# Kernel optimization log

Hardware: AMD Instinct MI355X
Metric: run time of the kernel (lower is better)

## Reference

```python
import jax, jax.numpy as jnp
import numpy as np

B, L, D = 8, 8192, 512
TARGET_RATIO = 1.0 / 6.0


def _normalize(v):
    # matches torch F.normalize(dim=-1, eps=1e-12)
    n = jnp.maximum(jnp.linalg.norm(v, axis=-1, keepdims=True), 1e-12)
    return v / n


def _downsample(x, b_hard):
    # vectorized stream compaction, padded to L (static upper bound of L_max)
    Bb, Ll, Dd = x.shape
    cnt = jnp.cumsum(b_hard.astype(jnp.int32), axis=1)
    pos = jnp.where(b_hard > 0.5, cnt - 1, Ll)          # non-selected -> dump slot L
    bidx = jnp.arange(Bb)[:, None]
    out = jnp.zeros((Bb, Ll + 1, Dd), x.dtype).at[bidx, pos].set(x)[:, :Ll]
    counts = cnt[:, -1]
    mask = jnp.arange(Ll)[None, :] < counts[:, None]
    return out, mask


def setup_inputs() -> dict:
    key = jax.random.key(0)
    k1, k2, k3 = jax.random.split(key, 3)
    x = jax.random.normal(k1, (B, L, D), jnp.float32)
    W_q = jax.random.normal(k2, (D, D), jnp.float32) / np.sqrt(D)
    W_k = jax.random.normal(k3, (D, D), jnp.float32) / np.sqrt(D)
    return {"x": x, "W_q": W_q, "W_k": W_k}


def reference(x, W_q, W_k):
    q = _normalize(jnp.einsum('bld,ed->ble', x, W_q))   # nn.Linear: x @ W.T
    k = _normalize(jnp.einsum('bld,ed->ble', x, W_k))
    k_prev = jnp.pad(k[:, :-1, :], ((0, 0), (1, 0), (0, 0)))
    cos_sim = jnp.sum(q * k_prev, axis=-1)               # (B, L)
    p = jnp.clip(0.5 * (1.0 - cos_sim), 0.0, 1.0)
    p = p.at[:, 0].set(1.0)                              # first position always boundary
    b_hard = (p >= 0.5).astype(x.dtype)
    N = 1.0 / TARGET_RATIO
    F_actual = jnp.mean(b_hard)
    G_actual = jnp.mean(p)
    ratio_loss = N / (N - 1.0) * ((N - 1.0) * F_actual * G_actual + (1.0 - F_actual) * (1.0 - G_actual))
    compressed, comp_mask = _downsample(x, b_hard)
    p_compressed, _ = _downsample(p[..., None], b_hard)
    p_compressed = p_compressed[..., 0]
    return (compressed, comp_mask, b_hard, p, p_compressed, ratio_loss)
```

## Files before the change

kernel.cpp:

```cpp
#include <hip/hip_runtime.h>
#include <hip/hip_bf16.h>
#include <math.h>

#define BB 8
#define LL 8192
#define DD 512
#define NROWS (BB * LL)

#define OUT_COMP   0
#define OUT_MASK   33554432
#define OUT_BHARD  33619968
#define OUT_P      33685504
#define OUT_PCOMP  33751040
#define OUT_LOSS   33816576

#define WS_FIXLIST 0
#define WS_FIXCNT  262144
#define WS_COUNTS  262148
#define WS_SUMP    262180
#define WS_SEL     262212
#define WS_SSK     524416
#define WS_SSQ     786560
#define WS_DOT     1048704
#define WS_WQH     1310848
#define WS_WKH     1835136

#define FIX_CAP 65536
#define FIX_TAU 1e-4f

typedef __attribute__((ext_vector_type(8))) _Float16 half8;
typedef __attribute__((ext_vector_type(4))) float f32x4;

static __device__ __forceinline__ void ld_g2l16(const void* g, void* l) {
  __builtin_amdgcn_global_load_lds(
      (const __attribute__((address_space(1))) void*)g,
      (__attribute__((address_space(3))) void*)l, 16, 0, 0);
}

__global__ __launch_bounds__(256) void wsplit(
    const float* __restrict__ Wq, const float* __restrict__ Wk,
    _Float16* __restrict__ wqh, _Float16* __restrict__ wkh,
    float* __restrict__ ssk, float* __restrict__ ssq,
    float* __restrict__ dotb, int* __restrict__ fixcnt) {
  const int t = blockIdx.x * 256 + threadIdx.x;
  if (t == 0) *fixcnt = 0;
  ssk[t] = 0.0f;
  ssq[t] = 0.0f;
  dotb[t] = 0.0f;

  const int m = t >> 15;
  const int c = t & 32767;
  const int kt = c >> 11;
  const int ct = (c >> 6) & 31;
  const int l = c & 63;
  const int n = l & 15;
  const int kblk = l >> 4;
  const int e = ct * 16 + n;
  const int d0 = kt * 32 + kblk * 8;
  const float* src = (m ? Wk : Wq) + (long)e * 512 + d0;
  _Float16* dh = (m ? wkh : wqh) + (long)c * 8;
  float4 v0 = *(const float4*)src;
  float4 v1 = *(const float4*)(src + 4);
  float av[8] = {v0.x, v0.y, v0.z, v0.w, v1.x, v1.y, v1.z, v1.w};
  half8 hi;
#pragma unroll
  for (int j = 0; j < 8; ++j) hi[j] = (_Float16)av[j];
  *(half8*)dh = hi;
}

__global__ __launch_bounds__(256, 2) void gemm_fused(
    const float* __restrict__ x,
    const _Float16* __restrict__ wqh, const _Float16* __restrict__ wkh,
    float* __restrict__ ssqOut, float* __restrict__ sskOut,
    float* __restrict__ dotOut,
    float* __restrict__ qedge, float* __restrict__ kedge) {
  __shared__ _Float16 smem[32768];
  _Float16* AH0 = smem;
  _Float16* AL0 = smem + 4096;
  _Float16* AH1 = smem + 8192;
  _Float16* AL1 = smem + 12288;
  _Float16* BQ0 = smem + 16384;
  _Float16* BK0 = smem + 20480;
  _Float16* BQ1 = smem + 24576;
  _Float16* BK1 = smem + 28672;

  const int tid = threadIdx.x;
  const int lane = tid & 63;
  const int w = tid >> 6;
  const int wrow = w & 1, wcol = w >> 1;
  const int g = lane >> 4, n = lane & 15;
  const int bx0 = blockIdx.x;
  const int bx = ((bx0 & 7) << 8) | (bx0 >> 3);
  const int rb = bx >> 2, cb = bx & 3;
  const long r0 = (long)rb * 128;

  const int arow = ((tid >> 6) << 4) | (tid & 15);
  const int akb = (tid >> 4) & 3;
  const float* ap = x + (r0 + arow) * 512 + akb * 8;

  f32x4 accq[4][4], acck[4][4];
#pragma unroll
  for (int mb = 0; mb < 4; ++mb)
#pragma unroll
    for (int nb = 0; nb < 4; ++nb) {
      accq[mb][nb] = (f32x4){0.f, 0.f, 0.f, 0.f};
      acck[mb][nb] = (f32x4){0.f, 0.f, 0.f, 0.f};
    }

#define STAGE_B(ktv, BQ_, BK_)                                              \
  do {                                                                      \
    const long bb = ((long)((ktv)*32 + cb * 8) << 9) + w * 1024 + lane * 8; \
    ld_g2l16(wqh + bb, (BQ_) + w * 1024);                                   \
    ld_g2l16(wqh + bb + 512, (BQ_) + w * 1024 + 512);                       \
    ld_g2l16(wkh + bb, (BK_) + w * 1024);                                   \
    ld_g2l16(wkh + bb + 512, (BK_) + w * 1024 + 512);                       \
  } while (0)

#define CONV_A(F0, F1, F2, F3, AH_, AL_)                                  \
  do {                                                                    \
    float av0[8] = {F0.x, F0.y, F0.z, F0.w, F1.x, F1.y, F1.z, F1.w};      \
    float av1[8] = {F2.x, F2.y, F2.z, F2.w, F3.x, F3.y, F3.z, F3.w};      \
    half8 h0, h1, l0, l1;                                                 \
    _Pragma("unroll") for (int j = 0; j < 8; ++j) {                       \
      _Float16 a = (_Float16)av0[j];                                      \
      h0[j] = a;                                                          \
      l0[j] = (_Float16)(av0[j] - (float)a);                              \
      _Float16 b = (_Float16)av1[j];                                      \
      h1[j] = b;                                                          \
      l1[j] = (_Float16)(av1[j] - (float)b);                              \
    }                                                                     \
    *(half8*)((AH_) + tid * 8) = h0;                                      \
    *(half8*)((AH_) + (tid + 256) * 8) = h1;                              \
    *(half8*)((AL_) + tid * 8) = l0;                                      \
    *(half8*)((AL_) + (tid + 256) * 8) = l1;                              \
  } while (0)

#define COMPUTE(AH_, AL_, BQ_, BK_)                                       \
  do {                                                                    \
    half8 ah[4], al[4], bq[4], bk[4];                                     \
    _Pragma("unroll") for (int nb = 0; nb < 4; ++nb) {                    \
      bq[nb] = *(const half8*)((BQ_) + ((wcol * 4 + nb) * 64 + lane) * 8);\
      bk[nb] = *(const half8*)((BK_) + ((wcol * 4 + nb) * 64 + lane) * 8);\
    }                                                                     \
    _Pragma("unroll") for (int mb = 0; mb < 4; ++mb) {                    \
      const int cm = wrow * 4 + mb;                                       \
      ah[mb] = *(const half8*)((AH_) + (cm * 64 + lane) * 8);             \
      al[mb] = *(const half8*)((AL_) + (cm * 64 + lane) * 8);             \
    }                                                                     \
    __builtin_amdgcn_s_setprio(1);                                        \
    _Pragma("unroll") for (int nb = 0; nb < 4; ++nb)                      \
        _Pragma("unroll") for (int mb = 0; mb < 4; ++mb) {                \
      accq[mb][nb] = __builtin_amdgcn_mfma_f32_16x16x32_f16(              \
          ah[mb], bq[nb], accq[mb][nb], 0, 0, 0);                         \
      acck[mb][nb] = __builtin_amdgcn_mfma_f32_16x16x32_f16(              \
          ah[mb], bk[nb], acck[mb][nb], 0, 0, 0);                         \
      accq[mb][nb] = __builtin_amdgcn_mfma_f32_16x16x32_f16(              \
          al[mb], bq[nb], accq[mb][nb], 0, 0, 0);                         \
      acck[mb][nb] = __builtin_amdgcn_mfma_f32_16x16x32_f16(              \
          al[mb], bk[nb], acck[mb][nb], 0, 0, 0);                        \
    }                                                                     \
    __builtin_amdgcn_s_setprio(0);                                        \
  } while (0)

#define BARRIER_CNT()                                       \
  do {                                                      \
    asm volatile("s_waitcnt vmcnt(4)" ::: "memory");        \
    asm volatile("s_waitcnt lgkmcnt(0)" ::: "memory");      \
    __builtin_amdgcn_sched_barrier(0);                      \
    __builtin_amdgcn_s_barrier();                           \
  } while (0)

#define FENCE() __builtin_amdgcn_sched_barrier(0)

  STAGE_B(0, BQ0, BK0);
  FENCE();
  float4 pa0 = *(const float4*)(ap);
  float4 pa1 = *(const float4*)(ap + 4);
  float4 pa2 = *(const float4*)(ap + 64 * 512);
  float4 pa3 = *(const float4*)(ap + 64 * 512 + 4);
  FENCE();
  CONV_A(pa0, pa1, pa2, pa3, AH0, AL0);
  float4 pb0 = *(const float4*)(ap + 32);
  float4 pb1 = *(const float4*)(ap + 32 + 4);
  float4 pb2 = *(const float4*)(ap + 32 + 64 * 512);
  float4 pb3 = *(const float4*)(ap + 32 + 64 * 512 + 4);
  FENCE();
  BARRIER_CNT();

  for (int i = 0; i < 8; ++i) {
    const int kt = 2 * i;
    STAGE_B(kt + 1, BQ1, BK1);
    FENCE();
    {
      const int ktn = (kt + 2 < 16) ? (kt + 2) : 15;
      const float* xp = ap + ktn * 32;
      pa0 = *(const float4*)(xp);
      pa1 = *(const float4*)(xp + 4);
      pa2 = *(const float4*)(xp + 64 * 512);
      pa3 = *(const float4*)(xp + 64 * 512 + 4);
    }
    FENCE();
    CONV_A(pb0, pb1, pb2, pb3, AH1, AL1);
    COMPUTE(AH0, AL0, BQ0, BK0);
    BARRIER_CNT();
    {
      const int ktn = (kt + 2 < 16) ? (kt + 2) : 15;
      STAGE_B(ktn, BQ0, BK0);
    }
    FENCE();
    {
      const int ktn = (kt + 3 < 16) ? (kt + 3) : 15;
      const float* xp2 = ap + ktn * 32;
      pb0 = *(const float4*)(xp2);
      pb1 = *(const float4*)(xp2 + 4);
      pb2 = *(const float4*)(xp2 + 64 * 512);
      pb3 = *(const float4*)(xp2 + 64 * 512 + 4);
    }
    FENCE();
    CONV_A(pa0, pa1, pa2, pa3, AH0, AL0);
    COMPUTE(AH1, AL1, BQ1, BK1);
    BARRIER_CNT();
  }

  asm volatile("s_waitcnt vmcnt(0)" ::: "memory");
  __builtin_amdgcn_sched_barrier(0);
  __syncthreads();

  _Float16* KX = smem;
  const int col0 = wcol * 64 + n;
  const int rbase = wrow * 64;
#pragma unroll
  for (int mb = 0; mb < 4; ++mb)
#pragma unroll
    for (int reg = 0; reg < 4; ++reg) {
      const int rl = rbase + mb * 16 + g * 4 + reg;
#pragma unroll
      for (int nb = 0; nb < 4; ++nb)
        KX[rl * 136 + col0 + nb * 16] = (_Float16)acck[mb][nb][reg];
    }
  __syncthreads();

  if (wrow == 1 && g == 3) {
#pragma unroll
    for (int nb = 0; nb < 4; ++nb)
      kedge[rb * 512 + cb * 128 + col0 + nb * 16] = acck[3][nb][3];
  }
  if (wrow == 0 && g == 0) {
#pragma unroll
    for (int nb = 0; nb < 4; ++nb)
      qedge[rb * 512 + cb * 128 + col0 + nb * 16] = accq[0][nb][0];
  }

#pragma unroll
  for (int mb = 0; mb < 4; ++mb) {
#pragma unroll
    for (int reg = 0; reg < 4; ++reg) {
      const int rl = rbase + mb * 16 + g * 4 + reg;
      const long row = r0 + rl;
      float sq = 0.f, sk = 0.f, dt = 0.f;
#pragma unroll
      for (int nb = 0; nb < 4; ++nb) {
        float qv = accq[mb][nb][reg];
        float kv = acck[mb][nb][reg];
        sq = fmaf(qv, qv, sq);
        sk = fmaf(kv, kv, sk);
        if (rl > 0) {
          float kp = (float)KX[(rl - 1) * 136 + col0 + nb * 16];
          dt = fmaf(qv, kp, dt);
        }
      }
#pragma unroll
      for (int m = 1; m < 16; m <<= 1) {
        sq += __shfl_xor(sq, m, 64);
        sk += __shfl_xor(sk, m, 64);
        dt += __shfl_xor(dt, m, 64);
      }
      if (n == 0) {
        atomicAdd(&ssqOut[row], sq);
        atomicAdd(&sskOut[row], sk);
        if (rl > 0) atomicAdd(&dotOut[row], dt);
      }
    }
  }
#undef STAGE_B
#undef CONV_A
#undef COMPUTE
#undef BARRIER_CNT
#undef FENCE
}

__global__ __launch_bounds__(64) void edgedot(
    const float* __restrict__ qedge, const float* __restrict__ kedge,
    float* __restrict__ dotOut) {
  const int rb = blockIdx.x;
  if (rb == 0) return;
  const long row = (long)rb * 128;
  if ((row & (LL - 1)) == 0) return;
  const int lane = threadIdx.x;
  float dt = 0.f;
#pragma unroll
  for (int c = lane; c < 512; c += 64)
    dt = fmaf(qedge[rb * 512 + c], kedge[(rb - 1) * 512 + c], dt);
#pragma unroll
  for (int m = 1; m < 64; m <<= 1) dt += __shfl_xor(dt, m, 64);
  if (lane == 0) dotOut[row] = dt;
}

__global__ __launch_bounds__(256) void combine(
    const float* __restrict__ ssq, const float* __restrict__ ssk,
    const float* __restrict__ dotb, float* __restrict__ dout,
    int* __restrict__ fixlist, int* __restrict__ fixcnt) {
  const int r = blockIdx.x * 256 + threadIdx.x;
  const int l = r & (LL - 1);
  float p;
  float cosv = 0.0f;
  if (l != 0) {
    float nq = fmaxf(sqrtf(ssq[r]), 1e-12f);
    float nk = fmaxf(sqrtf(ssk[r - 1]), 1e-12f);
    cosv = dotb[r] / (nq * nk);
    p = fminf(fmaxf(0.5f * (1.0f - cosv), 0.0f), 1.0f);
  } else {
    p = 1.0f;
  }
  dout[OUT_P + r] = p;
  dout[OUT_BHARD + r] = (p >= 0.5f) ? 1.0f : 0.0f;
  if (l != 0 && fabsf(cosv) < FIX_TAU) {
    int idx = atomicAdd(fixcnt, 1);
    if (idx < FIX_CAP) fixlist[idx] = r;
  }
}

__global__ __launch_bounds__(256) void fixup(
    const float* __restrict__ x, const float* __restrict__ Wq,
    const float* __restrict__ Wk, float* __restrict__ dout,
    const int* __restrict__ fixlist, const int* __restrict__ fixcnt) {
  __shared__ float xr[512], xp[512];
  __shared__ double red[3][256];
  const int t = threadIdx.x;
  int nfix = *fixcnt;
  if (nfix > FIX_CAP) nfix = FIX_CAP;

  for (int idx = blockIdx.x; idx < nfix; idx += gridDim.x) {
    const int r = fixlist[idx];
    for (int d = t; d < 512; d += 256) {
      xr[d] = x[(long)r * 512 + d];
      xp[d] = x[(long)(r - 1) * 512 + d];
    }
    __syncthreads();
    double ssq = 0.0, ssk = 0.0, dot = 0.0;
    for (int e = t; e < 512; e += 256) {
      const float* wq = Wq + (long)e * 512;
      const float* wk = Wk + (long)e * 512;
      double q = 0.0, k = 0.0;
      for (int d = 0; d < 512; ++d) {
        q = fma((double)xr[d], (double)wq[d], q);
        k = fma((double)xp[d], (double)wk[d], k);
      }
      ssq += q * q;
      ssk += k * k;
      dot += q * k;
    }
    red[0][t] = ssq;
    red[1][t] = ssk;
    red[2][t] = dot;
    __syncthreads();
    for (int s = 128; s > 0; s >>= 1) {
      if (t < s) {
        red[0][t] += red[0][t + s];
        red[1][t] += red[1][t + s];
        red[2][t] += red[2][t + s];
      }
      __syncthreads();
    }
    if (t == 0) {
      double nq = sqrt(red[0][0]);
      double nk = sqrt(red[1][0]);
      if (nq < 1e-12) nq = 1e-12;
      if (nk < 1e-12) nk = 1e-12;
      float c = (float)(red[2][0] / (nq * nk));
      float p = fminf(fmaxf(0.5f * (1.0f - c), 0.0f), 1.0f);
      dout[OUT_P + r] = p;
      dout[OUT_BHARD + r] = (p >= 0.5f) ? 1.0f : 0.0f;
    }
    __syncthreads();
  }
}

__global__ __launch_bounds__(256) void scanb(
    float* __restrict__ dout, int* __restrict__ sel,
    int* __restrict__ counts, float* __restrict__ sump) {
  __shared__ int wtot[4];
  __shared__ float wps[4];
  const int b = blockIdx.x;
  const int t = threadIdx.x;
  const int lane = t & 63, wv = t >> 6;
  const long base = (long)b * LL;

  int cnt = 0;
  float psum = 0.0f;
#pragma unroll 4
  for (int j = 0; j < 32; ++j) {
    int l = t * 32 + j;
    float bh = dout[OUT_BHARD + base + l];
    float pv = dout[OUT_P + base + l];
    cnt += (bh > 0.5f) ? 1 : 0;
    psum += pv;
  }
  int inc = cnt;
#pragma unroll
  for (int off = 1; off < 64; off <<= 1) {
    int u = __shfl_up(inc, off, 64);
    if (lane >= off) inc += u;
  }
  float ps = psum;
#pragma unroll
  for (int off = 1; off < 64; off <<= 1) ps += __shfl_xor(ps, off, 64);
  if (lane == 63) wtot[wv] = inc;
  if (lane == 0) wps[wv] = ps;
  __syncthreads();
  int wbase = 0, total = 0;
#pragma unroll
  for (int i = 0; i < 4; ++i) {
    int c = wtot[i];
    if (i < wv) wbase += c;
    total += c;
  }
  if (t == 0) {
    counts[b] = total;
    sump[b] = wps[0] + wps[1] + wps[2] + wps[3];
  }
  for (int j = 0; j < 32; ++j) {
    int l = t * 32 + j;
    dout[OUT_MASK + base + l] = (l < total) ? 1.0f : 0.0f;
    dout[OUT_PCOMP + base + l] = 0.0f;
  }
  __syncthreads();
  int pos = wbase + inc - cnt;
  for (int j = 0; j < 32; ++j) {
    int l = t * 32 + j;
    float bh = dout[OUT_BHARD + base + l];
    if (bh > 0.5f) {
      dout[OUT_PCOMP + base + pos] = dout[OUT_P + base + l];
      sel[base + pos] = l;
      ++pos;
    }
  }
}

__global__ void lossk(float* __restrict__ dout, const int* __restrict__ counts,
                      const float* __restrict__ sump) {
  if (threadIdx.x == 0 && blockIdx.x == 0) {
    float fc = 0.0f, gs = 0.0f;
    for (int b = 0; b < BB; ++b) {
      fc += (float)counts[b];
      gs += sump[b];
    }
    float F = fc / (float)NROWS;
    float G = gs / (float)NROWS;
    dout[OUT_LOSS] = 1.2f * (5.0f * F * G + (1.0f - F) * (1.0f - G));
  }
}

__global__ __launch_bounds__(128) void emit(
    const float* __restrict__ x, float* __restrict__ dout,
    const int* __restrict__ sel, const int* __restrict__ counts) {
  const long bid = blockIdx.x;
  const int b = (int)(bid >> 13);
  const int j = (int)(bid & (LL - 1));
  const int cnt = counts[b];
  float4 v = make_float4(0.0f, 0.0f, 0.0f, 0.0f);
  if (j < cnt) {
    const int l = sel[((long)b << 13) + j];
    v = *(const float4*)(x + (((long)b << 13) + l) * 512 + threadIdx.x * 4);
  }
  *(float4*)(dout + OUT_COMP + (((long)b << 13) + j) * 512 + threadIdx.x * 4) = v;
}

extern "C" void kernel_launch(void* const* d_in, const int* in_sizes, int n_in,
                              void* d_out, int out_size, void* d_ws,
                              size_t ws_size, hipStream_t stream) {
  const float* x = (const float*)d_in[0];
  const float* Wq = (const float*)d_in[1];
  const float* Wk = (const float*)d_in[2];
  float* out = (float*)d_out;
  char* ws = (char*)d_ws;

  int* fixlist = (int*)(ws + WS_FIXLIST);
  int* fixcnt = (int*)(ws + WS_FIXCNT);
  int* counts = (int*)(ws + WS_COUNTS);
  float* sump = (float*)(ws + WS_SUMP);
  int* sel = (int*)(ws + WS_SEL);
  float* ssk = (float*)(ws + WS_SSK);
  float* ssq = (float*)(ws + WS_SSQ);
  float* dotb = (float*)(ws + WS_DOT);
  _Float16* wqh = (_Float16*)(ws + WS_WQH);
  _Float16* wkh = (_Float16*)(ws + WS_WKH);

  float* kedge = (float*)(out + OUT_COMP);
  float* qedge = (float*)(out + OUT_COMP + 262144);

  wsplit<<<256, 256, 0, stream>>>(Wq, Wk, wqh, wkh, ssk, ssq, dotb, fixcnt);
  gemm_fused<<<2048, 256, 0, stream>>>(x, wqh, wkh, ssq, ssk, dotb, qedge, kedge);
  edgedot<<<512, 64, 0, stream>>>(qedge, kedge, dotb);
  combine<<<NROWS / 256, 256, 0, stream>>>(ssq, ssk, dotb, out, fixlist, fixcnt);
  fixup<<<512, 256, 0, stream>>>(x, Wq, Wk, out, fixlist, fixcnt);
  scanb<<<BB, 256, 0, stream>>>(out, sel, counts, sump);
  lossk<<<1, 64, 0, stream>>>(out, counts, sump);
  emit<<<NROWS, 128, 0, stream>>>(x, out, sel, counts);
}
```

Measured before the change: 468.7 us.

## Stage fp32 A tile via direct LDS loads, stream B weights from global into registers

The GEMM now copies raw fp32 x tiles into LDS with global_load_lds using an XOR-swizzled layout, and does the hi/lo fp16 split after reading from LDS in the compute step instead of before writing. The fp16 W tiles are no longer staged in LDS; each wave loads its B fragments straight from global memory into registers and prefetches the next k-tile's fragments between MFMA groups. The aim is to remove the register round trip and conversion stores on the A path and to cut LDS traffic and footprint for B. The trade-offs are extra global/L2 traffic for B, duplicated hi/lo conversion work across waves, and more dependence on vmcnt tuning. The fix-up tolerance is also tightened.

```diff
diff --git a/kernel.cpp b/kernel.cpp
--- a/kernel.cpp
+++ b/kernel.cpp
@@ -26,7 +26,7 @@
 #define WS_WKH     1835136
 
 #define FIX_CAP 65536
-#define FIX_TAU 1e-4f
+#define FIX_TAU 5e-5f
 
 typedef __attribute__((ext_vector_type(8))) _Float16 half8;
 typedef __attribute__((ext_vector_type(4))) float f32x4;
@@ -74,15 +74,9 @@
     float* __restrict__ ssqOut, float* __restrict__ sskOut,
     float* __restrict__ dotOut,
     float* __restrict__ qedge, float* __restrict__ kedge) {
-  __shared__ _Float16 smem[32768];
-  _Float16* AH0 = smem;
-  _Float16* AL0 = smem + 4096;
-  _Float16* AH1 = smem + 8192;
-  _Float16* AL1 = smem + 12288;
-  _Float16* BQ0 = smem + 16384;
-  _Float16* BK0 = smem + 20480;
-  _Float16* BQ1 = smem + 24576;
-  _Float16* BK1 = smem + 28672;
+  __shared__ float smemf[8704];
+  float* A0 = smemf;
+  float* A1 = smemf + 4096;
 
   const int tid = threadIdx.x;
   const int lane = tid & 63;
@@ -94,9 +88,18 @@
   const int rb = bx >> 2, cb = bx & 3;
   const long r0 = (long)rb * 128;
 
-  const int arow = ((tid >> 6) << 4) | (tid & 15);
-  const int akb = (tid >> 4) & 3;
-  const float* ap = x + (r0 + arow) * 512 + akb * 8;
+  const int srow = w * 32 + (lane >> 3);
+  const int scol = (((lane & 7) ^ (lane >> 3)) << 2);
+  const float* gsrc = x + (r0 + srow) * 512 + scol;
+
+  const int sw = (lane & 7) << 4;
+  const int kb0 = (lane >> 4) << 5;
+  const int o1 = kb0 ^ sw;
+  const int o2 = (kb0 + 16) ^ sw;
+  const int rdrow0 = wrow * 64 + (lane & 15);
+
+  const _Float16* bqb = wqh + ((long)((cb * 8 + wcol * 4) * 64 + lane)) * 8;
+  const _Float16* bkb = wkh + ((long)((cb * 8 + wcol * 4) * 64 + lane)) * 8;
 
   f32x4 accq[4][4], acck[4][4];
 #pragma unroll
@@ -107,64 +110,61 @@
       acck[mb][nb] = (f32x4){0.f, 0.f, 0.f, 0.f};
     }
 
-#define STAGE_B(ktv, BQ_, BK_)                                              \
-  do {                                                                      \
-    const long bb = ((long)((ktv)*32 + cb * 8) << 9) + w * 1024 + lane * 8; \
-    ld_g2l16(wqh + bb, (BQ_) + w * 1024);                                   \
-    ld_g2l16(wqh + bb + 512, (BQ_) + w * 1024 + 512);                       \
-    ld_g2l16(wkh + bb, (BK_) + w * 1024);                                   \
-    ld_g2l16(wkh + bb + 512, (BK_) + w * 1024 + 512);                       \
+  half8 bq[4], bk[4];
+
+#define STAGE_A(ktv, AB_)                                                 \
+  do {                                                                    \
+    _Pragma("unroll") for (int j = 0; j < 4; ++j)                         \
+        ld_g2l16(gsrc + j * 4096 + (ktv) * 32,                            \
+                 (char*)(AB_) + (w * 4 + j) * 1024);                      \
   } while (0)
 
-#define CONV_A(F0, F1, F2, F3, AH_, AL_)                                  \
+#define LOAD_B_ALL(ktv)                                                   \
   do {                                                                    \
-    float av0[8] = {F0.x, F0.y, F0.z, F0.w, F1.x, F1.y, F1.z, F1.w};      \
-    float av1[8] = {F2.x, F2.y, F2.z, F2.w, F3.x, F3.y, F3.z, F3.w};      \
-    half8 h0, h1, l0, l1;                                                 \
-    _Pragma("unroll") for (int j = 0; j < 8; ++j) {                       \
-      _Float16 a = (_Float16)av0[j];                                      \
-      h0[j] = a;                                                          \
-      l0[j] = (_Float16)(av0[j] - (float)a);                              \
-      _Float16 b = (_Float16)av1[j];                                      \
-      h1[j] = b;                                                          \
-      l1[j] = (_Float16)(av1[j] - (float)b);                              \
+    _Pragma("unroll") for (int nb = 0; nb < 4; ++nb) {                    \
+      bq[nb] = *(const half8*)(bqb + (long)(ktv)*16384 + nb * 512);       \
+      bk[nb] = *(const half8*)(bkb + (long)(ktv)*16384 + nb * 512);       \
     }                                                                     \
-    *(half8*)((AH_) + tid * 8) = h0;                                      \
-    *(half8*)((AH_) + (tid + 256) * 8) = h1;                              \
-    *(half8*)((AL_) + tid * 8) = l0;                                      \
-    *(half8*)((AL_) + (tid + 256) * 8) = l1;                              \
   } while (0)
 
-#define COMPUTE(AH_, AL_, BQ_, BK_)                                       \
+#define COMPUTE(AB_, KTN)                                                 \
   do {                                                                    \
-    half8 ah[4], al[4], bq[4], bk[4];                                     \
+    half8 ah[4], al[4];                                                   \
+    _Pragma("unroll") for (int mb = 0; mb < 4; ++mb) {                    \
+      const char* rp = (const char*)((AB_) + (rdrow0 + mb * 16) * 32);    \
+      float4 v0 = *(const float4*)(rp + o1);                              \
+      float4 v1 = *(const float4*)(rp + o2);                              \
+      float av[8] = {v0.x, v0.y, v0.z, v0.w, v1.x, v1.y, v1.z, v1.w};     \
+      half8 h, lo;                                                        \
+      _Pragma("unroll") for (int j = 0; j < 8; ++j) {                     \
+        _Float16 a = (_Float16)av[j];                                     \
+        h[j] = a;                                                         \
+        lo[j] = (_Float16)(av[j] - (float)a);                             \
+      }                                                                   \
+      ah[mb] = h;                                                         \
+      al[mb] = lo;                                                        \
+    }                                                                     \
     _Pragma("unroll") for (int nb = 0; nb < 4; ++nb) {                    \
-      bq[nb] = *(const half8*)((BQ_) + ((wcol * 4 + nb) * 64 + lane) * 8);\
-      bk[nb] = *(const half8*)((BK_) + ((wcol * 4 + nb) * 64 + lane) * 8);\
+      __builtin_amdgcn_s_setprio(1);                                      \
+      _Pragma("unroll") for (int mb = 0; mb < 4; ++mb) {                  \
+        accq[mb][nb] = __builtin_amdgcn_mfma_f32_16x16x32_f16(            \
+            ah[mb], bq[nb], accq[mb][nb], 0, 0, 0);                       \
+        acck[mb][nb] = __builtin_amdgcn_mfma_f32_16x16x32_f16(            \
+            ah[mb], bk[nb], acck[mb][nb], 0, 0, 0);                       \
+        accq[mb][nb] = __builtin_amdgcn_mfma_f32_16x16x32_f16(            \
+            al[mb], bq[nb], accq[mb][nb], 0, 0, 0);                       \
+        acck[mb][nb] = __builtin_amdgcn_mfma_f32_16x16x32_f16(            \
+            al[mb], bk[nb], acck[mb][nb], 0, 0, 0);                       \
+      }                                                                   \
+      __builtin_amdgcn_s_setprio(0);                                      \
+      bq[nb] = *(const half8*)(bqb + (long)(KTN)*16384 + nb * 512);       \
+      bk[nb] = *(const half8*)(bkb + (long)(KTN)*16384 + nb * 512);       \
     }                                                                     \
-    _Pragma("unroll") for (int mb = 0; mb < 4; ++mb) {                    \
-      const int cm = wrow * 4 + mb;                                       \
-      ah[mb] = *(const half8*)((AH_) + (cm * 64 + lane) * 8);             \
-      al[mb] = *(const half8*)((AL_) + (cm * 64 + lane) * 8);             \
-    }                                                                     \
-    __builtin_amdgcn_s_setprio(1);                                        \
-    _Pragma("unroll") for (int nb = 0; nb < 4; ++nb)                      \
-        _Pragma("unroll") for (int mb = 0; mb < 4; ++mb) {                \
-      accq[mb][nb] = __builtin_amdgcn_mfma_f32_16x16x32_f16(              \
-          ah[mb], bq[nb], accq[mb][nb], 0, 0, 0);                         \
-      acck[mb][nb] = __builtin_amdgcn_mfma_f32_16x16x32_f16(              \
-          ah[mb], bk[nb], acck[mb][nb], 0, 0, 0);                         \
-      accq[mb][nb] = __builtin_amdgcn_mfma_f32_16x16x32_f16(              \
-          al[mb], bq[nb], accq[mb][nb], 0, 0, 0);                         \
-      acck[mb][nb] = __builtin_amdgcn_mfma_f32_16x16x32_f16(              \
-          al[mb], bk[nb], acck[mb][nb], 0, 0, 0);                        \
-    }                                                                     \
-    __builtin_amdgcn_s_setprio(0);                                        \
   } while (0)
 
 #define BARRIER_CNT()                                       \
   do {                                                      \
-    asm volatile("s_waitcnt vmcnt(4)" ::: "memory");        \
+    asm volatile("s_waitcnt vmcnt(8)" ::: "memory");        \
     asm volatile("s_waitcnt lgkmcnt(0)" ::: "memory");      \
     __builtin_amdgcn_sched_barrier(0);                      \
     __builtin_amdgcn_s_barrier();                           \
@@ -172,53 +172,24 @@
 
 #define FENCE() __builtin_amdgcn_sched_barrier(0)
 
-  STAGE_B(0, BQ0, BK0);
+  STAGE_A(0, A0);
   FENCE();
-  float4 pa0 = *(const float4*)(ap);
-  float4 pa1 = *(const float4*)(ap + 4);
-  float4 pa2 = *(const float4*)(ap + 64 * 512);
-  float4 pa3 = *(const float4*)(ap + 64 * 512 + 4);
-  FENCE();
-  CONV_A(pa0, pa1, pa2, pa3, AH0, AL0);
-  float4 pb0 = *(const float4*)(ap + 32);
-  float4 pb1 = *(const float4*)(ap + 32 + 4);
-  float4 pb2 = *(const float4*)(ap + 32 + 64 * 512);
-  float4 pb3 = *(const float4*)(ap + 32 + 64 * 512 + 4);
+  LOAD_B_ALL(0);
   FENCE();
   BARRIER_CNT();
 
   for (int i = 0; i < 8; ++i) {
     const int kt = 2 * i;
-    STAGE_B(kt + 1, BQ1, BK1);
+    STAGE_A(kt + 1, A1);
     FENCE();
-    {
-      const int ktn = (kt + 2 < 16) ? (kt + 2) : 15;
-      const float* xp = ap + ktn * 32;
-      pa0 = *(const float4*)(xp);
-      pa1 = *(const float4*)(xp + 4);
-      pa2 = *(const float4*)(xp + 64 * 512);
-      pa3 = *(const float4*)(xp + 64 * 512 + 4);
-    }
-    FENCE();
-    CONV_A(pb0, pb1, pb2, pb3, AH1, AL1);
-    COMPUTE(AH0, AL0, BQ0, BK0);
+    COMPUTE(A0, kt + 1);
     BARRIER_CNT();
     {
       const int ktn = (kt + 2 < 16) ? (kt + 2) : 15;
-      STAGE_B(ktn, BQ0, BK0);
-    }
-    FENCE();
-    {
-      const int ktn = (kt + 3 < 16) ? (kt + 3) : 15;
-      const float* xp2 = ap + ktn * 32;
-      pb0 = *(const float4*)(xp2);
-      pb1 = *(const float4*)(xp2 + 4);
-      pb2 = *(const float4*)(xp2 + 64 * 512);
-      pb3 = *(const float4*)(xp2 + 64 * 512 + 4);
-    }
-    FENCE();
-    CONV_A(pa0, pa1, pa2, pa3, AH0, AL0);
-    COMPUTE(AH1, AL1, BQ1, BK1);
+      STAGE_A(ktn, A0);
+      FENCE();
+      COMPUTE(A1, ktn);
+    }
     BARRIER_CNT();
   }
 
@@ -226,7 +197,7 @@
   __builtin_amdgcn_sched_barrier(0);
   __syncthreads();
 
-  _Float16* KX = smem;
+  _Float16* KX = (_Float16*)smemf;
   const int col0 = wcol * 64 + n;
   const int rbase = wrow * 64;
 #pragma unroll
@@ -282,8 +253,8 @@
       }
     }
   }
-#undef STAGE_B
-#undef CONV_A
+#undef STAGE_A
+#undef LOAD_B_ALL
 #undef COMPUTE
 #undef BARRIER_CNT
 #undef FENCE
```

Result: faster. 457.2 us (-2.5%).
